# Optimization experiments

Hardware: AMD Instinct MI355X
Metric: run time of the kernel (lower is better)

## Reference

```python
import jax, jax.numpy as jnp
import numpy as np
import math

EPS_NORM = 1e-12
BN_EPS = 1e-5


def _l2norm(x):
    n = jnp.sqrt(jnp.sum(x * x, axis=-1, keepdims=True))
    return x / jnp.maximum(n, EPS_NORM)


def setup_inputs() -> dict:
    key = jax.random.key(0)
    ks = jax.random.split(key, 16)
    b, c, t, l = 16, 32, 16, 256
    s = 0.05
    return {
        "x": jax.random.normal(ks[0], (b, c, t, l), jnp.float32),
        "q_w": jax.random.normal(ks[1], (c, c), jnp.float32) * s,
        "q_b": jax.random.normal(ks[2], (c,), jnp.float32) * s,
        "k_w": jax.random.normal(ks[3], (c, c), jnp.float32) * s,
        "k_b": jax.random.normal(ks[4], (c,), jnp.float32) * s,
        "v_w": jax.random.normal(ks[5], (c, c), jnp.float32) * s,
        "v_b": jax.random.normal(ks[6], (c,), jnp.float32) * s,
        "m_w": jax.random.normal(ks[7], (c, c), jnp.float32) * s,
        "m_b": jax.random.normal(ks[8], (c,), jnp.float32) * s,
        "pre_prompt": jax.random.normal(ks[9], (1, c, 1, l), jnp.float32) * s,
        "conv_w": jax.random.normal(ks[10], (c, c, 9, 1), jnp.float32) * s,
        "conv_b": jax.random.normal(ks[11], (c,), jnp.float32) * s,
        "bn_gamma": jnp.ones((c,), jnp.float32),
        "bn_beta": jnp.zeros((c,), jnp.float32),
        "lin_w": jax.random.normal(ks[12], (l, l), jnp.float32) * s,
        "lin_b": jax.random.normal(ks[13], (l,), jnp.float32) * s,
        "atten_flag": 1,
    }


def reference(x, q_w, q_b, k_w, k_b, v_w, v_b, m_w, m_b, pre_prompt,
              conv_w, conv_b, bn_gamma, bn_beta, lin_w, lin_b, atten_flag):
    b, c, t, l = x.shape
    nh = 8
    hd = c // nh

    xp = jnp.transpose(x, (0, 2, 3, 1))  # (b,t,l,c)

    def heads(w, bias):
        h = xp @ w.T + bias
        h = h.reshape(b, t, l, nh, hd).transpose(0, 1, 3, 2, 4)  # (b,t,nh,l,hd)
        return _l2norm(h)

    q = heads(q_w, q_b)
    k = heads(k_w, k_b)
    v = heads(v_w, v_b)

    atten = jnp.einsum('bthld,bthmd->bthlm', q, k) / math.sqrt(hd)
    atten = jax.nn.softmax(atten, axis=-1)
    o = jnp.einsum('bthlm,bthmd->bthld', atten, v)  # (b,t,nh,l,hd)
    o = o.transpose(0, 1, 3, 2, 4).reshape(b, t, l, c)
    o = o @ m_w.T + m_b
    xo = jnp.transpose(o, (0, 3, 1, 2))  # (b,c,t,l)

    pre = jnp.broadcast_to(pre_prompt, (b, c, 1, l))
    con = jnp.concatenate([xo[:, :, :8], pre], axis=2)  # (b,c,9,l)

    # ConvNormAct: Conv2d (VALID, kernel (9,1)) + BatchNorm2d (batch stats) + ReLU
    h = jax.lax.conv_general_dilated(
        con, conv_w, window_strides=(1, 1), padding='VALID',
        dimension_numbers=('NCHW', 'OIHW', 'NCHW'))  # (b,c,1,l)
    h = h + conv_b[None, :, None, None]
    mean = jnp.mean(h, axis=(0, 2, 3), keepdims=True)
    var = jnp.var(h, axis=(0, 2, 3), keepdims=True)
    h = (h - mean) * jax.lax.rsqrt(var + BN_EPS)
    h = h * bn_gamma[None, :, None, None] + bn_beta[None, :, None, None]
    h = jax.nn.relu(h)

    p = h @ lin_w.T + lin_b  # Linear over token_len axis
    p = xo[:, :, 2:3] - p
    return jnp.concatenate([xo[:, :, :8], p], axis=2)  # (b,c,9,l)
```

## Files before the change

### kernel.cpp

```cpp
#include <hip/hip_runtime.h>
#include <hip/hip_bf16.h>


typedef __fp16 h2 __attribute__((ext_vector_type(2)));

#define O_OFF  0u
#define XO_OFF 2097152u
#define H_OFF  6291456u
#define S_OFF  6815744u

__device__ __forceinline__ int probe_f32(const unsigned short* graw) {
    return graw[0] == 0;
}
template<typename T> __device__ __forceinline__ float ldv(const T* p, long i);
template<> __device__ __forceinline__ float ldv<float>(const float* p, long i) {
    return p[i];
}
template<> __device__ __forceinline__ float ldv<__hip_bfloat16>(const __hip_bfloat16* p, long i) {
    return __bfloat162float(p[i]);
}
template<typename T> __device__ __forceinline__ void stv(T* p, size_t i, float v);
template<> __device__ __forceinline__ void stv<float>(float* p, size_t i, float v) {
    p[i] = v;
}
template<> __device__ __forceinline__ void stv<__hip_bfloat16>(__hip_bfloat16* p, size_t i, float v) {
    p[i] = __float2bfloat16(v);
}
__device__ __forceinline__ h2 pkh2(float a, float b) {
    return __builtin_amdgcn_cvt_pkrtz(a, b);
}
__device__ __forceinline__ float bflo(unsigned int u) {
    union { unsigned int i; float f; } c; c.i = u << 16; return c.f;
}
__device__ __forceinline__ float bfhi(unsigned int u) {
    union { unsigned int i; float f; } c; c.i = u & 0xffff0000u; return c.f;
}
#if __has_builtin(__builtin_amdgcn_fdot2)
__device__ __forceinline__ float fdot2(h2 a, h2 b, float c) {
    return __builtin_amdgcn_fdot2(a, b, c, false);
}
#else
__device__ __forceinline__ float fdot2(h2 a, h2 b, float c) {
    return fmaf((float)a[0], (float)b[0], fmaf((float)a[1], (float)b[1], c));
}
#endif
union KVrow { uint4 u; h2 h[4]; };

template<typename T>
__device__ __forceinline__ void attn_phase(
    const T* __restrict__ x,
    const T* __restrict__ qw, const T* __restrict__ qb,
    const T* __restrict__ kw, const T* __restrict__ kb,
    const T* __restrict__ vw, const T* __restrict__ vb,
    unsigned short* __restrict__ O, char* smem)
{
    uint4* KV = (uint4*)smem;
    float (*WL)[4][32] = (float (*)[4][32])(smem + 4096);
    float (*BL)[4]     = (float (*)[4])(smem + 5632);

    const int tid = threadIdx.x;
    const int blk = blockIdx.x;
    const int h = blk & 7, bt = blk >> 3;
    const int b = bt >> 3, t = bt & 7;
    const int h4 = h * 4;

    for (int e = tid; e < 384; e += 128) {
        int p = e >> 7, r = e & 127;
        const T* W = (p == 0) ? qw : ((p == 1) ? kw : vw);
        WL[p][r >> 5][r & 31] = ldv(W, (long)(h4 + (r >> 5)) * 32 + (r & 31));
    }
    if (tid < 12) {
        int p = tid >> 2, j = tid & 3;
        const T* B = (p == 0) ? qb : ((p == 1) ? kb : vb);
        BL[p][j] = ldv(B, h4 + j);
    }

    float xv0[32], xv1[32];
    #pragma unroll
    for (int c = 0; c < 32; c++) {
        const long xb = (((long)b * 32 + c) * 16 + t) * 256 + tid;
        xv0[c] = ldv(x, xb);
        xv1[c] = ldv(x, xb + 128);
    }
    __syncthreads();

    float4 pr0[3], pr1[3];
    #pragma unroll
    for (int p = 0; p < 3; p++) {
        float a0[4], a1[4];
        #pragma unroll
        for (int j = 0; j < 4; j++) { a0[j] = BL[p][j]; a1[j] = a0[j]; }
        #pragma unroll
        for (int c0 = 0; c0 < 32; c0 += 4) {
            float4 w0 = *(const float4*)&WL[p][0][c0];
            float4 w1 = *(const float4*)&WL[p][1][c0];
            float4 w2 = *(const float4*)&WL[p][2][c0];
            float4 w3 = *(const float4*)&WL[p][3][c0];
            const float* wj[4] = {(const float*)&w0, (const float*)&w1,
                                  (const float*)&w2, (const float*)&w3};
            #pragma unroll
            for (int cc = 0; cc < 4; cc++) {
                float x0 = xv0[c0+cc], x1 = xv1[c0+cc];
                #pragma unroll
                for (int j = 0; j < 4; j++) {
                    a0[j] = fmaf(x0, wj[j][cc], a0[j]);
                    a1[j] = fmaf(x1, wj[j][cc], a1[j]);
                }
            }
        }
        float s20 = a0[0]*a0[0] + a0[1]*a0[1] + a0[2]*a0[2] + a0[3]*a0[3];
        float s21 = a1[0]*a1[0] + a1[1]*a1[1] + a1[2]*a1[2] + a1[3]*a1[3];
        float i0 = 1.0f / fmaxf(sqrtf(s20), 1e-12f);
        float i1 = 1.0f / fmaxf(sqrtf(s21), 1e-12f);
        if (p == 0) { i0 *= 0.7213475204444817f; i1 *= 0.7213475204444817f; }
        pr0[p] = make_float4(a0[0]*i0, a0[1]*i0, a0[2]*i0, a0[3]*i0);
        pr1[p] = make_float4(a1[0]*i1, a1[1]*i1, a1[2]*i1, a1[3]*i1);
    }

    KVrow r0, r1;
    r0.h[0] = pkh2(pr0[1].x, pr0[1].y); r0.h[1] = pkh2(pr0[1].z, pr0[1].w);
    r0.h[2] = pkh2(pr0[2].x, pr0[2].y); r0.h[3] = pkh2(pr0[2].z, pr0[2].w);
    r1.h[0] = pkh2(pr1[1].x, pr1[1].y); r1.h[1] = pkh2(pr1[1].z, pr1[1].w);
    r1.h[2] = pkh2(pr1[2].x, pr1[2].y); r1.h[3] = pkh2(pr1[2].z, pr1[2].w);
    KV[tid]       = r0.u;
    KV[tid + 128] = r1.u;
    const h2 qa01 = pkh2(pr0[0].x, pr0[0].y), qa23 = pkh2(pr0[0].z, pr0[0].w);
    const h2 qb01 = pkh2(pr1[0].x, pr1[0].y), qb23 = pkh2(pr1[0].z, pr1[0].w);
    __syncthreads();

    h2 o01a = pkh2(0.f, 0.f), o23a = o01a, o01b = o01a, o23b = o01a;
    float den0 = 0.f, den1 = 0.f;
    #pragma unroll 8
    for (int m = 0; m < 256; m++) {
        KVrow kv; kv.u = KV[m];
        float sa = fdot2(qa01, kv.h[0], fdot2(qa23, kv.h[1], 0.0f));
        float sb = fdot2(qb01, kv.h[0], fdot2(qb23, kv.h[1], 0.0f));
        float ea = __builtin_amdgcn_exp2f(sa);
        float eb = __builtin_amdgcn_exp2f(sb);
        den0 += ea; den1 += eb;
        h2 epa = pkh2(ea, ea), epb = pkh2(eb, eb);
        o01a += epa * kv.h[2]; o23a += epa * kv.h[3];
        o01b += epb * kv.h[2]; o23b += epb * kv.h[3];
    }
    float i0 = 1.0f / den0, i1 = 1.0f / den1;
    h2 ia = pkh2(i0, i0), ib = pkh2(i1, i1);
    union { h2 h; unsigned int u; } c0, c1, c2, c3;
    c0.h = o01a * ia; c1.h = o23a * ia;
    c2.h = o01b * ib; c3.h = o23b * ib;
    *(uint2*)(O + ((size_t)bt * 256u + tid) * 32u + h4)       = make_uint2(c0.u, c1.u);
    *(uint2*)(O + ((size_t)bt * 256u + tid + 128) * 32u + h4) = make_uint2(c2.u, c3.u);
}

template<typename T>
__device__ __forceinline__ void mproj_phase(
    const unsigned short* __restrict__ O,
    const T* __restrict__ mw, const T* __restrict__ mb,
    T* __restrict__ out, float* __restrict__ xof, char* smem)
{
    float* sw = (float*)smem;
    float* sb = (float*)(smem + 4096);
    const int tid = threadIdx.x;
    const int blk = blockIdx.x;
    const int bt = blk >> 1, lhalf = blk & 1;
    const int b = bt >> 3, t = bt & 7;
    const int l = lhalf * 128 + tid;

    for (int e = tid; e < 1024; e += 128) sw[e] = ldv(mw, e);
    if (tid < 32) sb[tid] = ldv(mb, tid);

    float ov[32];
    const unsigned short* src = O + ((size_t)bt * 256u + l) * 32u;
    #pragma unroll
    for (int cc = 0; cc < 4; cc++) {
        union { uint4 u; h2 h[4]; } uu;
        uu.u = *(const uint4*)(src + cc * 8);
        #pragma unroll
        for (int j = 0; j < 4; j++) {
            ov[cc*8 + 2*j]     = (float)uu.h[j][0];
            ov[cc*8 + 2*j + 1] = (float)uu.h[j][1];
        }
    }
    __syncthreads();

    #pragma unroll 4
    for (int co = 0; co < 32; co++) {
        float s = sb[co];
        #pragma unroll
        for (int c0 = 0; c0 < 32; c0 += 4) {
            float4 w4 = *(const float4*)&sw[co * 32 + c0];
            s = fmaf(ov[c0+0], w4.x, s);
            s = fmaf(ov[c0+1], w4.y, s);
            s = fmaf(ov[c0+2], w4.z, s);
            s = fmaf(ov[c0+3], w4.w, s);
        }
        stv(out, (((size_t)b * 32 + co) * 9 + t) * 256u + l, s);
        xof[(((size_t)b * 32 + co) * 8 + t) * 256u + l] = s;
    }
}

template<typename T>
__device__ __forceinline__ void conv_phase(
    const float* __restrict__ xof, const T* __restrict__ pre,
    const T* __restrict__ cw, const T* __restrict__ cb,
    float* __restrict__ hout, float* __restrict__ s, char* smem)
{
    float* wl = (float*)smem;
    const int tid = threadIdx.x;
    const int blk = blockIdx.x;
    const int b = blk >> 4, cog = (blk >> 1) & 7, lhalf = blk & 1;
    const int co0 = cog * 4;
    const int l = lhalf * 128 + tid;

    for (int e = tid; e < 1152; e += 128) {
        int g = e & 3, r = e >> 2;
        wl[e] = ldv(cw, (long)(co0 + g) * 288 + r);
    }
    __syncthreads();

    float a0 = 0.f, a1 = 0.f, a2 = 0.f, a3 = 0.f;
    #pragma unroll 4
    for (int ci = 0; ci < 32; ci++) {
        const float* xp = xof + (((size_t)b * 32 + ci) * 8) * 256u + l;
        float v[9];
        #pragma unroll
        for (int kt = 0; kt < 8; kt++) v[kt] = xp[kt * 256];
        v[8] = ldv(pre, (long)ci * 256 + l);
        #pragma unroll
        for (int kt = 0; kt < 9; kt++) {
            float4 w4 = *(const float4*)&wl[(ci * 9 + kt) * 4];
            a0 = fmaf(v[kt], w4.x, a0);
            a1 = fmaf(v[kt], w4.y, a1);
            a2 = fmaf(v[kt], w4.z, a2);
            a3 = fmaf(v[kt], w4.w, a3);
        }
    }
    a0 += ldv(cb, co0+0); a1 += ldv(cb, co0+1);
    a2 += ldv(cb, co0+2); a3 += ldv(cb, co0+3);

    hout[((size_t)b * 32 + co0 + 0) * 256u + l] = a0;
    hout[((size_t)b * 32 + co0 + 1) * 256u + l] = a1;
    hout[((size_t)b * 32 + co0 + 2) * 256u + l] = a2;
    hout[((size_t)b * 32 + co0 + 3) * 256u + l] = a3;

    float acc[4] = {a0, a1, a2, a3};
    #pragma unroll
    for (int g = 0; g < 4; g++) {
        float sg = acc[g], sq = acc[g] * acc[g];
        #pragma unroll
        for (int off = 32; off > 0; off >>= 1) {
            sg += __shfl_down(sg, off, 64);
            sq += __shfl_down(sq, off, 64);
        }
        if ((tid & 63) == 0) {
            atomicAdd(&s[co0 + g], sg);
            atomicAdd(&s[32 + co0 + g], sq);
        }
    }
}

__device__ __forceinline__ float rowdot(const float* rp, const float* hn) {
    float acc = 0.f;
    #pragma unroll 4
    for (int i0 = 0; i0 < 256; i0 += 4) {
        float4 u = *(const float4*)(rp + i0);
        acc = fmaf(hn[i0+0], u.x, acc);
        acc = fmaf(hn[i0+1], u.y, acc);
        acc = fmaf(hn[i0+2], u.z, acc);
        acc = fmaf(hn[i0+3], u.w, acc);
    }
    return acc;
}
__device__ __forceinline__ float rowdot(const __hip_bfloat16* rp_, const float* hn) {
    const unsigned short* rp = (const unsigned short*)rp_;
    float acc = 0.f;
    #pragma unroll 2
    for (int i0 = 0; i0 < 256; i0 += 16) {
        uint4 u0 = *(const uint4*)(rp + i0);
        uint4 u1 = *(const uint4*)(rp + i0 + 8);
        unsigned int uu[8] = {u0.x, u0.y, u0.z, u0.w, u1.x, u1.y, u1.z, u1.w};
        #pragma unroll
        for (int j = 0; j < 8; j++) {
            acc = fmaf(hn[i0 + 2*j],     bflo(uu[j]), acc);
            acc = fmaf(hn[i0 + 2*j + 1], bfhi(uu[j]), acc);
        }
    }
    return acc;
}

template<typename T>
__device__ __forceinline__ void lin_phase(
    const float* __restrict__ hbuf, const float* __restrict__ sbuf,
    const T* __restrict__ gam, const T* __restrict__ bet,
    const T* __restrict__ lw, const T* __restrict__ lb,
    const float* __restrict__ xof, T* __restrict__ out, char* smem)
{
    float* hn = (float*)smem;
    const int tid = threadIdx.x;
    const int blk = blockIdx.x;
    const int b = blk >> 5, co = blk & 31;

    float mean = sbuf[co] * (1.0f / 4096.0f);
    float var  = fmaxf(sbuf[32 + co] * (1.0f / 4096.0f) - mean * mean, 0.0f);
    float sc = ldv(gam, co) * __frsqrt_rn(var + 1e-5f);
    float sh = ldv(bet, co) - mean * sc;

    const size_t hb = (size_t)blk * 256u;
    hn[tid]       = fmaxf(fmaf(hbuf[hb + tid], sc, sh), 0.0f);
    hn[tid + 128] = fmaxf(fmaf(hbuf[hb + tid + 128], sc, sh), 0.0f);
    __syncthreads();

    float acc0 = rowdot(lw + (size_t)tid * 256u, hn) + ldv(lb, tid);
    float acc1 = rowdot(lw + (size_t)(tid + 128) * 256u, hn) + ldv(lb, tid + 128);

    const size_t xb = (((size_t)b * 32 + co) * 8 + 2) * 256u;
    const size_t ob = (((size_t)b * 32 + co) * 9 + 8) * 256u;
    stv(out, ob + tid,       xof[xb + tid] - acc0);
    stv(out, ob + tid + 128, xof[xb + tid + 128] - acc1);
}

__global__ __launch_bounds__(128) void k_attn_s(
    const void* x, const void* qw, const void* qb, const void* kw,
    const void* kb, const void* vw, const void* vb,
    unsigned short* O, float* sbuf, const unsigned short* graw)
{
    __shared__ __align__(16) char smem[6144];
    if (blockIdx.x == 1023 && threadIdx.x < 64) sbuf[threadIdx.x] = 0.0f;
    if (probe_f32(graw))
        attn_phase<float>((const float*)x, (const float*)qw, (const float*)qb,
            (const float*)kw, (const float*)kb, (const float*)vw,
            (const float*)vb, O, smem);
    else
        attn_phase<__hip_bfloat16>((const __hip_bfloat16*)x,
            (const __hip_bfloat16*)qw, (const __hip_bfloat16*)qb,
            (const __hip_bfloat16*)kw, (const __hip_bfloat16*)kb,
            (const __hip_bfloat16*)vw, (const __hip_bfloat16*)vb, O, smem);
}
__global__ __launch_bounds__(128) void k_mproj_s(
    const unsigned short* O, const void* mw, const void* mb,
    void* out, float* xof, const unsigned short* graw)
{
    __shared__ __align__(16) char smem[6144];
    if (probe_f32(graw))
        mproj_phase<float>(O, (const float*)mw, (const float*)mb,
                           (float*)out, xof, smem);
    else
        mproj_phase<__hip_bfloat16>(O, (const __hip_bfloat16*)mw,
                                    (const __hip_bfloat16*)mb,
                                    (__hip_bfloat16*)out, xof, smem);
}
__global__ __launch_bounds__(128) void k_conv_s(
    const float* xof, const void* pre, const void* cw, const void* cb,
    float* hbuf, float* sbuf, const unsigned short* graw)
{
    __shared__ __align__(16) char smem[6144];
    if (probe_f32(graw))
        conv_phase<float>(xof, (const float*)pre, (const float*)cw,
                          (const float*)cb, hbuf, sbuf, smem);
    else
        conv_phase<__hip_bfloat16>(xof, (const __hip_bfloat16*)pre,
                                   (const __hip_bfloat16*)cw,
                                   (const __hip_bfloat16*)cb, hbuf, sbuf, smem);
}
__global__ __launch_bounds__(128) void k_lin_s(
    const float* hbuf, const float* sbuf, const void* gam, const void* bet,
    const void* lw, const void* lb, const float* xof, void* out,
    const unsigned short* graw)
{
    __shared__ __align__(16) char smem[6144];
    if (probe_f32(graw))
        lin_phase<float>(hbuf, sbuf, (const float*)gam, (const float*)bet,
                         (const float*)lw, (const float*)lb, xof,
                         (float*)out, smem);
    else
        lin_phase<__hip_bfloat16>(hbuf, sbuf, (const __hip_bfloat16*)gam,
                                  (const __hip_bfloat16*)bet,
                                  (const __hip_bfloat16*)lw,
                                  (const __hip_bfloat16*)lb, xof,
                                  (__hip_bfloat16*)out, smem);
}

extern "C" void kernel_launch(void* const* d_in, const int* in_sizes, int n_in,
                              void* d_out, int out_size, void* d_ws, size_t ws_size,
                              hipStream_t stream) {
    const void* x   = d_in[0];
    const void* qw  = d_in[1];  const void* qb  = d_in[2];
    const void* kw  = d_in[3];  const void* kb  = d_in[4];
    const void* vw  = d_in[5];  const void* vb  = d_in[6];
    const void* mw  = d_in[7];  const void* mb  = d_in[8];
    const void* pre = d_in[9];
    const void* cw  = d_in[10]; const void* cb  = d_in[11];
    const void* gam = d_in[12]; const void* bet = d_in[13];
    const void* lw  = d_in[14]; const void* lb  = d_in[15];
    const unsigned short* graw = (const unsigned short*)d_in[12];

    unsigned short* Obuf = (unsigned short*)((char*)d_ws + O_OFF);
    float* xof  = (float*)((char*)d_ws + XO_OFF);
    float* hbuf = (float*)((char*)d_ws + H_OFF);
    float* sbuf = (float*)((char*)d_ws + S_OFF);

    k_attn_s <<<1024, 128, 0, stream>>>(x, qw, qb, kw, kb, vw, vb,
                                        Obuf, sbuf, graw);
    k_mproj_s<<<256,  128, 0, stream>>>(Obuf, mw, mb, d_out, xof, graw);
    k_conv_s <<<256,  128, 0, stream>>>(xof, pre, cw, cb, hbuf, sbuf, graw);
    k_lin_s  <<<512,  128, 0, stream>>>(hbuf, sbuf, gam, bet, lw, lb,
                                        xof, d_out, graw);
}
```

Before: 183.6 us.

## Shrink attention blocks to one wavefront with four query rows per thread

The attention kernel now runs 64 threads per block instead of 128, and each thread handles four query/key rows instead of two. The QKV projection, normalization, KV staging and the softmax-weighted loop are restructured to match, so each LDS read of a KV row is reused across four queries. This cuts LDS read traffic per query and drops the cross-wave barrier cost within a block. In exchange each thread holds more registers (128 x values plus 48 accumulators), and the grid has half as many threads in flight, which lowers latency hiding.

```diff
diff --git a/kernel.cpp b/kernel.cpp
--- a/kernel.cpp
+++ b/kernel.cpp
@@ -64,7 +64,7 @@
     const int b = bt >> 3, t = bt & 7;
     const int h4 = h * 4;
 
-    for (int e = tid; e < 384; e += 128) {
+    for (int e = tid; e < 384; e += 64) {
         int p = e >> 7, r = e & 127;
         const T* W = (p == 0) ? qw : ((p == 1) ? kw : vw);
         WL[p][r >> 5][r & 31] = ldv(W, (long)(h4 + (r >> 5)) * 32 + (r & 31));
@@ -75,80 +75,88 @@
         BL[p][j] = ldv(B, h4 + j);
     }
 
-    float xv0[32], xv1[32];
+    float xv[32][4];
+    const long xbase = (((long)b * 32) * 16 + t) * 256 + tid;
     #pragma unroll
     for (int c = 0; c < 32; c++) {
-        const long xb = (((long)b * 32 + c) * 16 + t) * 256 + tid;
-        xv0[c] = ldv(x, xb);
-        xv1[c] = ldv(x, xb + 128);
+        const long xb = xbase + (long)c * 4096;
+        #pragma unroll
+        for (int r = 0; r < 4; r++) xv[c][r] = ldv(x, xb + 64 * r);
     }
     __syncthreads();
 
-    float4 pr0[3], pr1[3];
-    #pragma unroll
-    for (int p = 0; p < 3; p++) {
-        float a0[4], a1[4];
-        #pragma unroll
-        for (int j = 0; j < 4; j++) { a0[j] = BL[p][j]; a1[j] = a0[j]; }
-        #pragma unroll
-        for (int c0 = 0; c0 < 32; c0 += 4) {
-            float4 w0 = *(const float4*)&WL[p][0][c0];
-            float4 w1 = *(const float4*)&WL[p][1][c0];
-            float4 w2 = *(const float4*)&WL[p][2][c0];
-            float4 w3 = *(const float4*)&WL[p][3][c0];
-            const float* wj[4] = {(const float*)&w0, (const float*)&w1,
-                                  (const float*)&w2, (const float*)&w3};
+    float acc[3][4][4];
+    #pragma unroll
+    for (int p = 0; p < 3; p++)
+        #pragma unroll
+        for (int j = 0; j < 4; j++) {
+            float bj = BL[p][j];
             #pragma unroll
-            for (int cc = 0; cc < 4; cc++) {
-                float x0 = xv0[c0+cc], x1 = xv1[c0+cc];
+            for (int r = 0; r < 4; r++) acc[p][j][r] = bj;
+        }
+    #pragma unroll
+    for (int c = 0; c < 32; c++) {
+        #pragma unroll
+        for (int p = 0; p < 3; p++)
+            #pragma unroll
+            for (int j = 0; j < 4; j++) {
+                float w = WL[p][j][c];
                 #pragma unroll
-                for (int j = 0; j < 4; j++) {
-                    a0[j] = fmaf(x0, wj[j][cc], a0[j]);
-                    a1[j] = fmaf(x1, wj[j][cc], a1[j]);
-                }
+                for (int r = 0; r < 4; r++)
+                    acc[p][j][r] = fmaf(xv[c][r], w, acc[p][j][r]);
             }
-        }
-        float s20 = a0[0]*a0[0] + a0[1]*a0[1] + a0[2]*a0[2] + a0[3]*a0[3];
-        float s21 = a1[0]*a1[0] + a1[1]*a1[1] + a1[2]*a1[2] + a1[3]*a1[3];
-        float i0 = 1.0f / fmaxf(sqrtf(s20), 1e-12f);
-        float i1 = 1.0f / fmaxf(sqrtf(s21), 1e-12f);
-        if (p == 0) { i0 *= 0.7213475204444817f; i1 *= 0.7213475204444817f; }
-        pr0[p] = make_float4(a0[0]*i0, a0[1]*i0, a0[2]*i0, a0[3]*i0);
-        pr1[p] = make_float4(a1[0]*i1, a1[1]*i1, a1[2]*i1, a1[3]*i1);
-    }
-
-    KVrow r0, r1;
-    r0.h[0] = pkh2(pr0[1].x, pr0[1].y); r0.h[1] = pkh2(pr0[1].z, pr0[1].w);
-    r0.h[2] = pkh2(pr0[2].x, pr0[2].y); r0.h[3] = pkh2(pr0[2].z, pr0[2].w);
-    r1.h[0] = pkh2(pr1[1].x, pr1[1].y); r1.h[1] = pkh2(pr1[1].z, pr1[1].w);
-    r1.h[2] = pkh2(pr1[2].x, pr1[2].y); r1.h[3] = pkh2(pr1[2].z, pr1[2].w);
-    KV[tid]       = r0.u;
-    KV[tid + 128] = r1.u;
-    const h2 qa01 = pkh2(pr0[0].x, pr0[0].y), qa23 = pkh2(pr0[0].z, pr0[0].w);
-    const h2 qb01 = pkh2(pr1[0].x, pr1[0].y), qb23 = pkh2(pr1[0].z, pr1[0].w);
+    }
+
+    h2 qv[4][2];
+    #pragma unroll
+    for (int r = 0; r < 4; r++) {
+        float pr[3][4];
+        #pragma unroll
+        for (int p = 0; p < 3; p++) {
+            float s2 = acc[p][0][r]*acc[p][0][r] + acc[p][1][r]*acc[p][1][r]
+                     + acc[p][2][r]*acc[p][2][r] + acc[p][3][r]*acc[p][3][r];
+            float inv = 1.0f / fmaxf(sqrtf(s2), 1e-12f);
+            if (p == 0) inv *= 0.7213475204444817f;
+            #pragma unroll
+            for (int j = 0; j < 4; j++) pr[p][j] = acc[p][j][r] * inv;
+        }
+        qv[r][0] = pkh2(pr[0][0], pr[0][1]);
+        qv[r][1] = pkh2(pr[0][2], pr[0][3]);
+        KVrow rr;
+        rr.h[0] = pkh2(pr[1][0], pr[1][1]); rr.h[1] = pkh2(pr[1][2], pr[1][3]);
+        rr.h[2] = pkh2(pr[2][0], pr[2][1]); rr.h[3] = pkh2(pr[2][2], pr[2][3]);
+        KV[tid + 64 * r] = rr.u;
+    }
     __syncthreads();
 
-    h2 o01a = pkh2(0.f, 0.f), o23a = o01a, o01b = o01a, o23b = o01a;
-    float den0 = 0.f, den1 = 0.f;
+    h2 o01[4], o23[4];
+    float den[4];
+    #pragma unroll
+    for (int r = 0; r < 4; r++) {
+        o01[r] = pkh2(0.f, 0.f); o23[r] = o01[r]; den[r] = 0.f;
+    }
     #pragma unroll 8
     for (int m = 0; m < 256; m++) {
         KVrow kv; kv.u = KV[m];
-        float sa = fdot2(qa01, kv.h[0], fdot2(qa23, kv.h[1], 0.0f));
-        float sb = fdot2(qb01, kv.h[0], fdot2(qb23, kv.h[1], 0.0f));
-        float ea = __builtin_amdgcn_exp2f(sa);
-        float eb = __builtin_amdgcn_exp2f(sb);
-        den0 += ea; den1 += eb;
-        h2 epa = pkh2(ea, ea), epb = pkh2(eb, eb);
-        o01a += epa * kv.h[2]; o23a += epa * kv.h[3];
-        o01b += epb * kv.h[2]; o23b += epb * kv.h[3];
-    }
-    float i0 = 1.0f / den0, i1 = 1.0f / den1;
-    h2 ia = pkh2(i0, i0), ib = pkh2(i1, i1);
-    union { h2 h; unsigned int u; } c0, c1, c2, c3;
-    c0.h = o01a * ia; c1.h = o23a * ia;
-    c2.h = o01b * ib; c3.h = o23b * ib;
-    *(uint2*)(O + ((size_t)bt * 256u + tid) * 32u + h4)       = make_uint2(c0.u, c1.u);
-    *(uint2*)(O + ((size_t)bt * 256u + tid + 128) * 32u + h4) = make_uint2(c2.u, c3.u);
+        #pragma unroll
+        for (int r = 0; r < 4; r++) {
+            float s = fdot2(qv[r][0], kv.h[0], fdot2(qv[r][1], kv.h[1], 0.0f));
+            float e = __builtin_amdgcn_exp2f(s);
+            den[r] += e;
+            h2 ep = pkh2(e, e);
+            o01[r] += ep * kv.h[2];
+            o23[r] += ep * kv.h[3];
+        }
+    }
+    #pragma unroll
+    for (int r = 0; r < 4; r++) {
+        float inv = 1.0f / den[r];
+        h2 iv = pkh2(inv, inv);
+        union { h2 h; unsigned int u; } c0, c1;
+        c0.h = o01[r] * iv; c1.h = o23[r] * iv;
+        *(uint2*)(O + ((size_t)bt * 256u + tid + 64 * r) * 32u + h4)
+            = make_uint2(c0.u, c1.u);
+    }
 }
 
 template<typename T>
@@ -318,13 +326,13 @@
     stv(out, ob + tid + 128, xof[xb + tid + 128] - acc1);
 }
 
-__global__ __launch_bounds__(128) void k_attn_s(
+__global__ __launch_bounds__(64, 2) void k_attn_s(
     const void* x, const void* qw, const void* qb, const void* kw,
     const void* kb, const void* vw, const void* vb,
     unsigned short* O, float* sbuf, const unsigned short* graw)
 {
     __shared__ __align__(16) char smem[6144];
-    if (blockIdx.x == 1023 && threadIdx.x < 64) sbuf[threadIdx.x] = 0.0f;
+    if (blockIdx.x == 1023) sbuf[threadIdx.x] = 0.0f;
     if (probe_f32(graw))
         attn_phase<float>((const float*)x, (const float*)qw, (const float*)qb,
             (const float*)kw, (const float*)kb, (const float*)vw,
@@ -398,7 +406,7 @@
     float* hbuf = (float*)((char*)d_ws + H_OFF);
     float* sbuf = (float*)((char*)d_ws + S_OFF);
 
-    k_attn_s <<<1024, 128, 0, stream>>>(x, qw, qb, kw, kb, vw, vb,
+    k_attn_s <<<1024, 64,  0, stream>>>(x, qw, qb, kw, kb, vw, vb,
                                         Obuf, sbuf, graw);
     k_mproj_s<<<256,  128, 0, stream>>>(Obuf, mw, mb, d_out, xof, graw);
     k_conv_s <<<256,  128, 0, stream>>>(xof, pre, cw, cb, hbuf, sbuf, graw);
```

New measurement: 216.7 us. 18.1% more time.

## Split attention key range across two blocks and merge partial sums in projection

Applied to the files above, without the earlier changes.

The attention kernel now launches twice as many blocks. Each block handles half of the 256 key/value rows, still computes Q for all 256 queries, and writes unnormalized partial outputs plus softmax denominators in fp32. The m-projection kernel sums the two partials and divides by the combined denominator. This is valid because there is no max subtraction, since the L2-normalized scores are bounded. The conv kernel also splits output channels into pairs to double its grid. The aim is more parallelism, at the cost of recomputing the QKV projection twice and a larger fp32 intermediate buffer written to and read from global memory.

```diff
diff --git a/kernel.cpp b/kernel.cpp
--- a/kernel.cpp
+++ b/kernel.cpp
@@ -4,10 +4,10 @@
 
 typedef __fp16 h2 __attribute__((ext_vector_type(2)));
 
-#define O_OFF  0u
-#define XO_OFF 2097152u
-#define H_OFF  6291456u
-#define S_OFF  6815744u
+#define P_OFF  0u
+#define XO_OFF 10485760u
+#define H_OFF  14680064u
+#define S_OFF  15204352u
 
 __device__ __forceinline__ int probe_f32(const unsigned short* graw) {
     return graw[0] == 0;
@@ -52,15 +52,17 @@
     const T* __restrict__ qw, const T* __restrict__ qb,
     const T* __restrict__ kw, const T* __restrict__ kb,
     const T* __restrict__ vw, const T* __restrict__ vb,
-    unsigned short* __restrict__ O, char* smem)
+    float* __restrict__ P, char* smem)
 {
     uint4* KV = (uint4*)smem;
-    float (*WL)[4][32] = (float (*)[4][32])(smem + 4096);
-    float (*BL)[4]     = (float (*)[4])(smem + 5632);
-
-    const int tid = threadIdx.x;
-    const int blk = blockIdx.x;
-    const int h = blk & 7, bt = blk >> 3;
+    float (*WL)[4][32] = (float (*)[4][32])(smem + 2048);
+    float (*BL)[4]     = (float (*)[4])(smem + 3584);
+
+    const int tid  = threadIdx.x;
+    const int blk  = blockIdx.x;
+    const int half = blk & 1;
+    const int h    = (blk >> 1) & 7;
+    const int bt   = blk >> 4;
     const int b = bt >> 3, t = bt & 7;
     const int h4 = h * 4;
 
@@ -91,22 +93,14 @@
         #pragma unroll
         for (int j = 0; j < 4; j++) { a0[j] = BL[p][j]; a1[j] = a0[j]; }
         #pragma unroll
-        for (int c0 = 0; c0 < 32; c0 += 4) {
-            float4 w0 = *(const float4*)&WL[p][0][c0];
-            float4 w1 = *(const float4*)&WL[p][1][c0];
-            float4 w2 = *(const float4*)&WL[p][2][c0];
-            float4 w3 = *(const float4*)&WL[p][3][c0];
-            const float* wj[4] = {(const float*)&w0, (const float*)&w1,
-                                  (const float*)&w2, (const float*)&w3};
-            #pragma unroll
-            for (int cc = 0; cc < 4; cc++) {
-                float x0 = xv0[c0+cc], x1 = xv1[c0+cc];
-                #pragma unroll
-                for (int j = 0; j < 4; j++) {
-                    a0[j] = fmaf(x0, wj[j][cc], a0[j]);
-                    a1[j] = fmaf(x1, wj[j][cc], a1[j]);
-                }
-            }
+        for (int c = 0; c < 32; c++) {
+            float w0 = WL[p][0][c], w1 = WL[p][1][c];
+            float w2 = WL[p][2][c], w3 = WL[p][3][c];
+            float x0 = xv0[c], x1 = xv1[c];
+            a0[0] = fmaf(x0, w0, a0[0]); a1[0] = fmaf(x1, w0, a1[0]);
+            a0[1] = fmaf(x0, w1, a0[1]); a1[1] = fmaf(x1, w1, a1[1]);
+            a0[2] = fmaf(x0, w2, a0[2]); a1[2] = fmaf(x1, w2, a1[2]);
+            a0[3] = fmaf(x0, w3, a0[3]); a1[3] = fmaf(x1, w3, a1[3]);
         }
         float s20 = a0[0]*a0[0] + a0[1]*a0[1] + a0[2]*a0[2] + a0[3]*a0[3];
         float s21 = a1[0]*a1[0] + a1[1]*a1[1] + a1[2]*a1[2] + a1[3]*a1[3];
@@ -117,13 +111,12 @@
         pr1[p] = make_float4(a1[0]*i1, a1[1]*i1, a1[2]*i1, a1[3]*i1);
     }
 
-    KVrow r0, r1;
-    r0.h[0] = pkh2(pr0[1].x, pr0[1].y); r0.h[1] = pkh2(pr0[1].z, pr0[1].w);
-    r0.h[2] = pkh2(pr0[2].x, pr0[2].y); r0.h[3] = pkh2(pr0[2].z, pr0[2].w);
-    r1.h[0] = pkh2(pr1[1].x, pr1[1].y); r1.h[1] = pkh2(pr1[1].z, pr1[1].w);
-    r1.h[2] = pkh2(pr1[2].x, pr1[2].y); r1.h[3] = pkh2(pr1[2].z, pr1[2].w);
-    KV[tid]       = r0.u;
-    KV[tid + 128] = r1.u;
+    float4 kk = half ? pr1[1] : pr0[1];
+    float4 vv = half ? pr1[2] : pr0[2];
+    KVrow rr;
+    rr.h[0] = pkh2(kk.x, kk.y); rr.h[1] = pkh2(kk.z, kk.w);
+    rr.h[2] = pkh2(vv.x, vv.y); rr.h[3] = pkh2(vv.z, vv.w);
+    KV[tid] = rr.u;
     const h2 qa01 = pkh2(pr0[0].x, pr0[0].y), qa23 = pkh2(pr0[0].z, pr0[0].w);
     const h2 qb01 = pkh2(pr1[0].x, pr1[0].y), qb23 = pkh2(pr1[0].z, pr1[0].w);
     __syncthreads();
@@ -131,7 +124,7 @@
     h2 o01a = pkh2(0.f, 0.f), o23a = o01a, o01b = o01a, o23b = o01a;
     float den0 = 0.f, den1 = 0.f;
     #pragma unroll 8
-    for (int m = 0; m < 256; m++) {
+    for (int m = 0; m < 128; m++) {
         KVrow kv; kv.u = KV[m];
         float sa = fdot2(qa01, kv.h[0], fdot2(qa23, kv.h[1], 0.0f));
         float sb = fdot2(qb01, kv.h[0], fdot2(qb23, kv.h[1], 0.0f));
@@ -142,18 +135,23 @@
         o01a += epa * kv.h[2]; o23a += epa * kv.h[3];
         o01b += epb * kv.h[2]; o23b += epb * kv.h[3];
     }
-    float i0 = 1.0f / den0, i1 = 1.0f / den1;
-    h2 ia = pkh2(i0, i0), ib = pkh2(i1, i1);
-    union { h2 h; unsigned int u; } c0, c1, c2, c3;
-    c0.h = o01a * ia; c1.h = o23a * ia;
-    c2.h = o01b * ib; c3.h = o23b * ib;
-    *(uint2*)(O + ((size_t)bt * 256u + tid) * 32u + h4)       = make_uint2(c0.u, c1.u);
-    *(uint2*)(O + ((size_t)bt * 256u + tid + 128) * 32u + h4) = make_uint2(c2.u, c3.u);
+
+    float* base = P + (((size_t)(bt * 2 + half) * 8 + h) * 5) * 256u;
+    base[0 * 256 + tid] = (float)o01a[0];
+    base[1 * 256 + tid] = (float)o01a[1];
+    base[2 * 256 + tid] = (float)o23a[0];
+    base[3 * 256 + tid] = (float)o23a[1];
+    base[4 * 256 + tid] = den0;
+    base[0 * 256 + tid + 128] = (float)o01b[0];
+    base[1 * 256 + tid + 128] = (float)o01b[1];
+    base[2 * 256 + tid + 128] = (float)o23b[0];
+    base[3 * 256 + tid + 128] = (float)o23b[1];
+    base[4 * 256 + tid + 128] = den1;
 }
 
 template<typename T>
 __device__ __forceinline__ void mproj_phase(
-    const unsigned short* __restrict__ O,
+    const float* __restrict__ P,
     const T* __restrict__ mw, const T* __restrict__ mb,
     T* __restrict__ out, float* __restrict__ xof, char* smem)
 {
@@ -169,16 +167,15 @@
     if (tid < 32) sb[tid] = ldv(mb, tid);
 
     float ov[32];
-    const unsigned short* src = O + ((size_t)bt * 256u + l) * 32u;
     #pragma unroll
-    for (int cc = 0; cc < 4; cc++) {
-        union { uint4 u; h2 h[4]; } uu;
-        uu.u = *(const uint4*)(src + cc * 8);
-        #pragma unroll
-        for (int j = 0; j < 4; j++) {
-            ov[cc*8 + 2*j]     = (float)uu.h[j][0];
-            ov[cc*8 + 2*j + 1] = (float)uu.h[j][1];
-        }
+    for (int h = 0; h < 8; h++) {
+        const float* p0 = P + (((size_t)(bt * 2 + 0) * 8 + h) * 5) * 256u + l;
+        const float* p1 = P + (((size_t)(bt * 2 + 1) * 8 + h) * 5) * 256u + l;
+        float den = p0[4 * 256] + p1[4 * 256];
+        float inv = 1.0f / den;
+        #pragma unroll
+        for (int j = 0; j < 4; j++)
+            ov[h * 4 + j] = (p0[j * 256] + p1[j * 256]) * inv;
     }
     __syncthreads();
 
@@ -207,45 +204,49 @@
     float* wl = (float*)smem;
     const int tid = threadIdx.x;
     const int blk = blockIdx.x;
-    const int b = blk >> 4, cog = (blk >> 1) & 7, lhalf = blk & 1;
-    const int co0 = cog * 4;
+    const int b = blk >> 5, cog2 = (blk >> 1) & 15, lhalf = blk & 1;
+    const int co0 = cog2 * 2;
     const int l = lhalf * 128 + tid;
 
-    for (int e = tid; e < 1152; e += 128) {
-        int g = e & 3, r = e >> 2;
+    for (int e = tid; e < 576; e += 128) {
+        int g = e & 1, r = e >> 1;
         wl[e] = ldv(cw, (long)(co0 + g) * 288 + r);
     }
     __syncthreads();
 
-    float a0 = 0.f, a1 = 0.f, a2 = 0.f, a3 = 0.f;
-    #pragma unroll 4
-    for (int ci = 0; ci < 32; ci++) {
-        const float* xp = xof + (((size_t)b * 32 + ci) * 8) * 256u + l;
-        float v[9];
-        #pragma unroll
-        for (int kt = 0; kt < 8; kt++) v[kt] = xp[kt * 256];
-        v[8] = ldv(pre, (long)ci * 256 + l);
+    float a0 = 0.f, a1 = 0.f;
+    #pragma unroll 2
+    for (int ci = 0; ci < 32; ci += 2) {
+        const float* xpA = xof + (((size_t)b * 32 + ci) * 8) * 256u + l;
+        const float* xpB = xpA + 8 * 256;
+        float va[9], vb[9];
+        #pragma unroll
+        for (int kt = 0; kt < 8; kt++) {
+            va[kt] = xpA[kt * 256];
+            vb[kt] = xpB[kt * 256];
+        }
+        va[8] = ldv(pre, (long)ci * 256 + l);
+        vb[8] = ldv(pre, (long)(ci + 1) * 256 + l);
         #pragma unroll
         for (int kt = 0; kt < 9; kt++) {
-            float4 w4 = *(const float4*)&wl[(ci * 9 + kt) * 4];
-            a0 = fmaf(v[kt], w4.x, a0);
-            a1 = fmaf(v[kt], w4.y, a1);
-            a2 = fmaf(v[kt], w4.z, a2);
-            a3 = fmaf(v[kt], w4.w, a3);
-        }
-    }
-    a0 += ldv(cb, co0+0); a1 += ldv(cb, co0+1);
-    a2 += ldv(cb, co0+2); a3 += ldv(cb, co0+3);
+            float2 wA = *(const float2*)&wl[(ci * 9 + kt) * 2];
+            float2 wB = *(const float2*)&wl[((ci + 1) * 9 + kt) * 2];
+            a0 = fmaf(va[kt], wA.x, a0);
+            a1 = fmaf(va[kt], wA.y, a1);
+            a0 = fmaf(vb[kt], wB.x, a0);
+            a1 = fmaf(vb[kt], wB.y, a1);
+        }
+    }
+    a0 += ldv(cb, co0 + 0);
+    a1 += ldv(cb, co0 + 1);
 
     hout[((size_t)b * 32 + co0 + 0) * 256u + l] = a0;
     hout[((size_t)b * 32 + co0 + 1) * 256u + l] = a1;
-    hout[((size_t)b * 32 + co0 + 2) * 256u + l] = a2;
-    hout[((size_t)b * 32 + co0 + 3) * 256u + l] = a3;
-
-    float acc[4] = {a0, a1, a2, a3};
+
+    float acc2[2] = {a0, a1};
     #pragma unroll
-    for (int g = 0; g < 4; g++) {
-        float sg = acc[g], sq = acc[g] * acc[g];
+    for (int g = 0; g < 2; g++) {
+        float sg = acc2[g], sq = acc2[g] * acc2[g];
         #pragma unroll
         for (int off = 32; off > 0; off >>= 1) {
             sg += __shfl_down(sg, off, 64);
@@ -318,33 +319,33 @@
     stv(out, ob + tid + 128, xof[xb + tid + 128] - acc1);
 }
 
-__global__ __launch_bounds__(128) void k_attn_s(
+__global__ __launch_bounds__(128, 2) void k_attn_s(
     const void* x, const void* qw, const void* qb, const void* kw,
     const void* kb, const void* vw, const void* vb,
-    unsigned short* O, float* sbuf, const unsigned short* graw)
-{
-    __shared__ __align__(16) char smem[6144];
-    if (blockIdx.x == 1023 && threadIdx.x < 64) sbuf[threadIdx.x] = 0.0f;
+    float* P, float* sbuf, const unsigned short* graw)
+{
+    __shared__ __align__(16) char smem[4096];
+    if (blockIdx.x == 2047 && threadIdx.x < 64) sbuf[threadIdx.x] = 0.0f;
     if (probe_f32(graw))
         attn_phase<float>((const float*)x, (const float*)qw, (const float*)qb,
             (const float*)kw, (const float*)kb, (const float*)vw,
-            (const float*)vb, O, smem);
+            (const float*)vb, P, smem);
     else
         attn_phase<__hip_bfloat16>((const __hip_bfloat16*)x,
             (const __hip_bfloat16*)qw, (const __hip_bfloat16*)qb,
             (const __hip_bfloat16*)kw, (const __hip_bfloat16*)kb,
-            (const __hip_bfloat16*)vw, (const __hip_bfloat16*)vb, O, smem);
+            (const __hip_bfloat16*)vw, (const __hip_bfloat16*)vb, P, smem);
 }
 __global__ __launch_bounds__(128) void k_mproj_s(
-    const unsigned short* O, const void* mw, const void* mb,
+    const float* P, const void* mw, const void* mb,
     void* out, float* xof, const unsigned short* graw)
 {
-    __shared__ __align__(16) char smem[6144];
+    __shared__ __align__(16) char smem[4608];
     if (probe_f32(graw))
-        mproj_phase<float>(O, (const float*)mw, (const float*)mb,
+        mproj_phase<float>(P, (const float*)mw, (const float*)mb,
                            (float*)out, xof, smem);
     else
-        mproj_phase<__hip_bfloat16>(O, (const __hip_bfloat16*)mw,
+        mproj_phase<__hip_bfloat16>(P, (const __hip_bfloat16*)mw,
                                     (const __hip_bfloat16*)mb,
                                     (__hip_bfloat16*)out, xof, smem);
 }
@@ -352,7 +353,7 @@
     const float* xof, const void* pre, const void* cw, const void* cb,
     float* hbuf, float* sbuf, const unsigned short* graw)
 {
-    __shared__ __align__(16) char smem[6144];
+    __shared__ __align__(16) char smem[2304];
     if (probe_f32(graw))
         conv_phase<float>(xof, (const float*)pre, (const float*)cw,
                           (const float*)cb, hbuf, sbuf, smem);
@@ -366,7 +367,7 @@
     const void* lw, const void* lb, const float* xof, void* out,
     const unsigned short* graw)
 {
-    __shared__ __align__(16) char smem[6144];
+    __shared__ __align__(16) char smem[1024];
     if (probe_f32(graw))
         lin_phase<float>(hbuf, sbuf, (const float*)gam, (const float*)bet,
                          (const float*)lw, (const float*)lb, xof,
@@ -393,15 +394,15 @@
     const void* lw  = d_in[14]; const void* lb  = d_in[15];
     const unsigned short* graw = (const unsigned short*)d_in[12];
 
-    unsigned short* Obuf = (unsigned short*)((char*)d_ws + O_OFF);
+    float* Pbuf = (float*)((char*)d_ws + P_OFF);
     float* xof  = (float*)((char*)d_ws + XO_OFF);
     float* hbuf = (float*)((char*)d_ws + H_OFF);
     float* sbuf = (float*)((char*)d_ws + S_OFF);
 
-    k_attn_s <<<1024, 128, 0, stream>>>(x, qw, qb, kw, kb, vw, vb,
-                                        Obuf, sbuf, graw);
-    k_mproj_s<<<256,  128, 0, stream>>>(Obuf, mw, mb, d_out, xof, graw);
-    k_conv_s <<<256,  128, 0, stream>>>(xof, pre, cw, cb, hbuf, sbuf, graw);
+    k_attn_s <<<2048, 128, 0, stream>>>(x, qw, qb, kw, kb, vw, vb,
+                                        Pbuf, sbuf, graw);
+    k_mproj_s<<<256,  128, 0, stream>>>(Pbuf, mw, mb, d_out, xof, graw);
+    k_conv_s <<<512,  128, 0, stream>>>(xof, pre, cw, cb, hbuf, sbuf, graw);
     k_lin_s  <<<512,  128, 0, stream>>>(hbuf, sbuf, gam, bet, lw, lb,
                                         xof, d_out, graw);
 }
```

Measured after the change: 183.6 us. Within noise of the previous version (+0.0%).
